# Kernel optimization log

Measured on AMD Instinct MI355X. Metric: run time of the kernel, lower is better.

The kernel has to match this reference:

```python
import jax, jax.numpy as jnp
import numpy as np

B, L = 4, 2048
D_MODEL, D_STATE, D_CONV, N_BLOCKS = 128, 16, 8, 6
EXPAND = 2
D_INNER = EXPAND * D_MODEL          # 256
DT_RANK = (D_MODEL + 15) // 16      # 8
CONV_K = 7                          # pre_conv kernel


def setup_inputs() -> dict:
    key = jax.random.key(0)
    ks = jax.random.split(key, 10)
    f = lambda k, s: jax.random.normal(k, s, jnp.float32)
    sc = 0.02
    A_init = jnp.broadcast_to(
        jnp.log(jnp.arange(1, D_STATE + 1, dtype=jnp.float32)),
        (N_BLOCKS, D_INNER, D_STATE)) + 0.0
    return {
        "x": f(ks[0], (B, L, 1)),
        "pre_conv_w": f(ks[1], (D_MODEL, 1, CONV_K)) * sc,
        "pre_conv_b": jnp.zeros((D_MODEL,), jnp.float32),
        "ln_w": jnp.ones((N_BLOCKS, D_MODEL), jnp.float32),
        "ln_b": jnp.zeros((N_BLOCKS, D_MODEL), jnp.float32),
        "W_in": f(ks[2], (N_BLOCKS, 2 * D_INNER, D_MODEL)) * sc,
        "conv_w": f(ks[3], (N_BLOCKS, D_INNER, 1, D_CONV)) * sc,  # depthwise OIH
        "conv_b": jnp.zeros((N_BLOCKS, D_INNER), jnp.float32),
        "W_x": f(ks[4], (N_BLOCKS, DT_RANK + 2 * D_STATE, D_INNER)) * sc,
        "W_dt": f(ks[5], (N_BLOCKS, D_INNER, DT_RANK)) * sc,
        "b_dt": jnp.full((N_BLOCKS, D_INNER), -4.6, jnp.float32),  # softplus ~ 0.01
        "A_log": A_init,
        "D_skip": jnp.ones((N_BLOCKS, D_INNER), jnp.float32),
        "W_out": f(ks[6], (N_BLOCKS, D_MODEL, D_INNER)) * sc,
        "out_w": f(ks[7], (1, D_MODEL)) * sc,
        "out_b": jnp.zeros((1,), jnp.float32),
    }


def _layernorm(x, w, b, eps=1e-5):
    m = jnp.mean(x, axis=-1, keepdims=True)
    v = jnp.mean(jnp.square(x - m), axis=-1, keepdims=True)
    return (x - m) * jax.lax.rsqrt(v + eps) * w + b


def _mamba(x, W_in, cw, cb, W_x, W_dt, b_dt, A_log, D_skip, W_out):
    # x: (B, L, D_MODEL)
    xz = jnp.einsum('bld,ed->ble', x, W_in)            # (B,L,2E)
    xi, z = jnp.split(xz, 2, axis=-1)
    # depthwise causal conv over time
    xc = jax.lax.conv_general_dilated(
        xi.transpose(0, 2, 1), cw, window_strides=(1,),
        padding=[(D_CONV - 1, 0)],
        dimension_numbers=('NCH', 'OIH', 'NCH'),
        feature_group_count=D_INNER) + cb[None, :, None]
    xc = jax.nn.silu(xc).transpose(0, 2, 1)            # (B,L,E)
    dbl = jnp.einsum('ble,re->blr', xc, W_x)
    dt = dbl[..., :DT_RANK]
    Bm = dbl[..., DT_RANK:DT_RANK + D_STATE]           # (B,L,N)
    Cm = dbl[..., DT_RANK + D_STATE:]                  # (B,L,N)
    delta = jax.nn.softplus(jnp.einsum('blr,er->ble', dt, W_dt) + b_dt)
    A = -jnp.exp(A_log)                                # (E,N)

    def step(h, inp):
        d, b, c, u = inp                               # (B,E),(B,N),(B,N),(B,E)
        h = h * jnp.exp(d[..., None] * A) + (d * u)[..., None] * b[:, None, :]
        return h, jnp.einsum('ben,bn->be', h, c)

    h0 = jnp.zeros((x.shape[0], D_INNER, D_STATE), x.dtype)
    xs = (delta.transpose(1, 0, 2), Bm.transpose(1, 0, 2),
          Cm.transpose(1, 0, 2), xc.transpose(1, 0, 2))
    _, ys = jax.lax.scan(step, h0, xs)                 # ys: (L,B,E)
    y = ys.transpose(1, 0, 2) + D_skip * xc
    y = y * jax.nn.silu(z)
    return jnp.einsum('ble,de->bld', y, W_out)


def reference(x, pre_conv_w, pre_conv_b, ln_w, ln_b, W_in, conv_w, conv_b,
              W_x, W_dt, b_dt, A_log, D_skip, W_out, out_w, out_b):
    # pre_conv (1 -> d_model), SAME padding, then exact GELU
    h = jax.lax.conv_general_dilated(
        x.transpose(0, 2, 1), pre_conv_w, window_strides=(1,),
        padding=[(CONV_K // 2, CONV_K // 2)],
        dimension_numbers=('NCH', 'OIH', 'NCH')) + pre_conv_b[None, :, None]
    h = jax.nn.gelu(h, approximate=False).transpose(0, 2, 1)  # (B,L,D)

    def block(carry, p):
        lw, lb, Wi, cw, cb, Wx, Wdt, bdt, Alog, Dsk, Wo = p
        y = _mamba(_layernorm(carry, lw, lb), Wi, cw, cb, Wx, Wdt, bdt, Alog, Dsk, Wo)
        return carry + y, None                         # dropout is identity (eval)

    h, _ = jax.lax.scan(block, h, (ln_w, ln_b, W_in, conv_w, conv_b,
                                   W_x, W_dt, b_dt, A_log, D_skip, W_out))
    return (jnp.einsum('bld,od->blo', h, out_w) + out_b)[..., 0]  # (B,L)
```

## Files before the change

### kernel.cpp

```cpp
#include <hip/hip_runtime.h>
#include <hip/hip_bf16.h>
#include <math.h>

#define BB 4
#define LL 2048
#define DM 128
#define DI 256
#define DS 16
#define DTR 8
#define NB 6
#define KPRE 7
#define KC 8
#define NC 64
#define CT 32
#define BL (BB*LL)
#define SU 4

typedef __attribute__((ext_vector_type(8))) short short8v;
typedef __attribute__((ext_vector_type(4))) float f32x4;

__global__ void k_preconv_gelu(const float* __restrict__ x,
                               const float* __restrict__ w,
                               const float* __restrict__ bias,
                               float* __restrict__ h,
                               const float* __restrict__ Wi,
                               const float* __restrict__ Wo,
                               __hip_bfloat16* __restrict__ wi,
                               __hip_bfloat16* __restrict__ wo) {
    int tid = blockIdx.x * blockDim.x + threadIdx.x;
    int d = tid & (DM - 1);
    int l = (tid >> 7) & (LL - 1);
    int b = tid >> 18;
    float acc = bias[d];
#pragma unroll
    for (int k = 0; k < KPRE; ++k) {
        int pos = l + k - 3;
        float xv = (pos >= 0 && pos < LL) ? x[b * LL + pos] : 0.f;
        acc = fmaf(xv, w[d * KPRE + k], acc);
    }
    h[tid] = 0.5f * acc * (1.f + erff(acc * 0.70710678118654752f));
    if (tid < NB * 2 * DI * DM) wi[tid] = __float2bfloat16(Wi[tid]);
    if (tid < NB * DM * DI)     wo[tid] = __float2bfloat16(Wo[tid]);
}

__global__ __launch_bounds__(256) void k_ln_gemm1(const float* __restrict__ h,
                                                  const float* __restrict__ lw,
                                                  const float* __restrict__ lb,
                                                  const __hip_bfloat16* __restrict__ W,
                                                  float* __restrict__ xz) {
    __shared__ __hip_bfloat16 As[128 * 128];
    int wave = threadIdx.x >> 6;
    int lane = threadIdx.x & 63;
    int mBase = blockIdx.x * 128;
    int nBase = blockIdx.y * 128;
    for (int it = 0; it < 32; ++it) {
        int row = wave * 32 + it;
        int t = mBase + row;
        float v0 = h[t * DM + lane];
        float v1 = h[t * DM + lane + 64];
        float s = v0 + v1;
#pragma unroll
        for (int off = 32; off; off >>= 1) s += __shfl_xor(s, off);
        float mean = s * (1.f / 128.f);
        float d0 = v0 - mean, d1 = v1 - mean;
        float q = d0 * d0 + d1 * d1;
#pragma unroll
        for (int off = 32; off; off >>= 1) q += __shfl_xor(q, off);
        float rstd = rsqrtf(q * (1.f / 128.f) + 1e-5f);
        int sw = (row & 7) << 3;
        As[row * 128 + (lane ^ sw)]        = __float2bfloat16(d0 * rstd * lw[lane] + lb[lane]);
        As[row * 128 + ((lane + 64) ^ sw)] = __float2bfloat16(d1 * rstd * lw[lane + 64] + lb[lane + 64]);
    }
    __syncthreads();
    int wm = wave & 1, wn = wave >> 1;
    int r  = lane & 15;
    int kh = lane >> 4;
    f32x4 acc[4][4] = {};
    for (int k0 = 0; k0 < DM; k0 += 32) {
        short8v af[4], bf[4];
#pragma unroll
        for (int i = 0; i < 4; ++i) {
            int row = wm * 64 + i * 16 + r;
            int cbk = (k0 >> 3) + kh;
            af[i] = *(const short8v*)&As[row * 128 + ((cbk ^ (row & 7)) << 3)];
            bf[i] = *(const short8v*)&W[(size_t)(nBase + wn * 64 + i * 16 + r) * DM + k0 + kh * 8];
        }
#pragma unroll
        for (int i = 0; i < 4; ++i)
#pragma unroll
            for (int j = 0; j < 4; ++j)
                acc[i][j] = __builtin_amdgcn_mfma_f32_16x16x32_bf16(af[i], bf[j], acc[i][j], 0, 0, 0);
    }
#pragma unroll
    for (int i = 0; i < 4; ++i)
#pragma unroll
        for (int j = 0; j < 4; ++j)
#pragma unroll
            for (int rg = 0; rg < 4; ++rg) {
                size_t off = (size_t)(mBase + wm * 64 + i * 16 + kh * 4 + rg) * (2 * DI)
                           + nBase + wn * 64 + j * 16 + r;
                xz[off] = acc[i][j][rg];
            }
}

__global__ __launch_bounds__(256) void k_gemm2_mfma(const __hip_bfloat16* __restrict__ A,
                                                    const __hip_bfloat16* __restrict__ W,
                                                    float* __restrict__ C) {
    int wave = threadIdx.x >> 6;
    int lane = threadIdx.x & 63;
    int wm = wave & 1, wn = wave >> 1;
    int mBase = blockIdx.x * 128 + wm * 64;
    int nBase = wn * 64;
    int r  = lane & 15;
    int kh = lane >> 4;
    f32x4 acc[4][4] = {};
    for (int k0 = 0; k0 < DI; k0 += 32) {
        short8v af[4], bf[4];
#pragma unroll
        for (int i = 0; i < 4; ++i) {
            af[i] = *(const short8v*)&A[(size_t)(mBase + i * 16 + r) * DI + k0 + kh * 8];
            bf[i] = *(const short8v*)&W[(size_t)(nBase + i * 16 + r) * DI + k0 + kh * 8];
        }
#pragma unroll
        for (int i = 0; i < 4; ++i)
#pragma unroll
            for (int j = 0; j < 4; ++j)
                acc[i][j] = __builtin_amdgcn_mfma_f32_16x16x32_bf16(af[i], bf[j], acc[i][j], 0, 0, 0);
    }
#pragma unroll
    for (int i = 0; i < 4; ++i)
#pragma unroll
        for (int j = 0; j < 4; ++j)
#pragma unroll
            for (int rg = 0; rg < 4; ++rg) {
                size_t off = (size_t)(mBase + i * 16 + kh * 4 + rg) * DM + nBase + j * 16 + r;
                C[off] += acc[i][j][rg];
            }
}

__global__ __launch_bounds__(256) void k_conv_wx(const float* __restrict__ xz,
                                                 const float* __restrict__ cw,
                                                 const float* __restrict__ cbs,
                                                 const float* __restrict__ Wx,
                                                 const float* __restrict__ Wdt,
                                                 const float* __restrict__ bdt,
                                                 float* __restrict__ xc,
                                                 float* __restrict__ BC,
                                                 float* __restrict__ delta) {
    int lane = threadIdx.x & 63;
    int t = blockIdx.x * 4 + (threadIdx.x >> 6);
    int tl = t & (LL - 1);
    int b = t >> 11;
    float xv[4];
#pragma unroll
    for (int j = 0; j < 4; ++j) {
        int e = lane + 64 * j;
        float4 cw0 = *(const float4*)&cw[e * KC];
        float4 cw1 = *(const float4*)&cw[e * KC + 4];
        float wts[8] = {cw0.x, cw0.y, cw0.z, cw0.w, cw1.x, cw1.y, cw1.z, cw1.w};
        float acc = cbs[e];
#pragma unroll
        for (int k = 0; k < KC; ++k) {
            int pos = tl + k - (KC - 1);
            float v = (pos >= 0) ? xz[((size_t)(b * LL + pos) << 9) + e] : 0.f;
            acc = fmaf(v, wts[k], acc);
        }
        xv[j] = acc / (1.f + __expf(-acc));
        xc[((size_t)t << 8) + e] = xv[j];
    }
    float dt[8];
    float bcv = 0.f;
#pragma unroll
    for (int o = 0; o < 40; ++o) {
        const float* w = &Wx[o * DI];
        float s = xv[0] * w[lane];
        s = fmaf(xv[1], w[lane + 64], s);
        s = fmaf(xv[2], w[lane + 128], s);
        s = fmaf(xv[3], w[lane + 192], s);
#pragma unroll
        for (int off = 32; off; off >>= 1) s += __shfl_xor(s, off);
        if (o < 8) dt[o] = s;
        else if (lane == o - 8) bcv = s;
    }
    if (lane < 32) BC[((size_t)t << 5) + lane] = bcv;
#pragma unroll
    for (int j = 0; j < 4; ++j) {
        int e = lane + 64 * j;
        float s = bdt[e];
#pragma unroll
        for (int r = 0; r < 8; ++r) s = fmaf(dt[r], Wdt[e * 8 + r], s);
        delta[((size_t)t << 8) + e] = fmaxf(s, 0.f) + log1pf(__expf(-fabsf(s)));
    }
}

__global__ __launch_bounds__(256) void k_scan1(const float* __restrict__ delta,
                                               const float* __restrict__ xc,
                                               const float* __restrict__ BC,
                                               const float* __restrict__ A_log,
                                               float* __restrict__ P,
                                               float* __restrict__ hend) {
    int blk = blockIdx.x;
    int eg = blk & 3;
    int c = (blk >> 2) & (NC - 1);
    int b = blk >> 8;
    int tid = threadIdx.x;
    int e = eg * 64 + (tid >> 2);
    int ng = tid & 3;
    float4 al = *(const float4*)&A_log[e * DS + 4 * ng];
    float Aen[4] = {-__expf(al.x), -__expf(al.y), -__expf(al.z), -__expf(al.w)};
    float h[4] = {}, Pl[4] = {1.f, 1.f, 1.f, 1.f};
    int base = b * LL + c * CT;
    const float* dp = delta + (size_t)base * DI + e;
    const float* up = xc + (size_t)base * DI + e;
    const float* bp = BC + (size_t)base * 32 + 4 * ng;
    for (int l0 = 0; l0 < CT; l0 += SU) {
        float d[SU], u[SU];
        float4 bm[SU];
#pragma unroll
        for (int j = 0; j < SU; ++j) {
            d[j]  = dp[(l0 + j) * DI];
            u[j]  = up[(l0 + j) * DI];
            bm[j] = *(const float4*)&bp[(l0 + j) * 32];
        }
#pragma unroll
        for (int j = 0; j < SU; ++j) {
            float du = d[j] * u[j];
            float a0 = __expf(d[j] * Aen[0]);
            float a1 = __expf(d[j] * Aen[1]);
            float a2 = __expf(d[j] * Aen[2]);
            float a3 = __expf(d[j] * Aen[3]);
            h[0] = fmaf(h[0], a0, du * bm[j].x);
            h[1] = fmaf(h[1], a1, du * bm[j].y);
            h[2] = fmaf(h[2], a2, du * bm[j].z);
            h[3] = fmaf(h[3], a3, du * bm[j].w);
            Pl[0] *= a0; Pl[1] *= a1; Pl[2] *= a2; Pl[3] *= a3;
        }
    }
    size_t oidx = (((size_t)(b * NC + c)) * DI + e) * DS + 4 * ng;
    *(float4*)&P[oidx]    = make_float4(Pl[0], Pl[1], Pl[2], Pl[3]);
    *(float4*)&hend[oidx] = make_float4(h[0], h[1], h[2], h[3]);
}

__global__ void k_scan_carry(const float* __restrict__ P,
                             const float* __restrict__ hend,
                             float* __restrict__ hin) {
    int tid = blockIdx.x * blockDim.x + threadIdx.x;
    int n = tid & 15;
    int e = (tid >> 4) & 255;
    int b = tid >> 12;
    float carry = 0.f;
    for (int c = 0; c < NC; ++c) {
        size_t idx = (((size_t)(b * NC + c)) * DI + e) * DS + n;
        hin[idx] = carry;
        carry = fmaf(P[idx], carry, hend[idx]);
    }
}

__global__ __launch_bounds__(256) void k_scan3(const float* __restrict__ delta,
                                               const float* __restrict__ xc,
                                               const float* __restrict__ BC,
                                               const float* __restrict__ A_log,
                                               const float* __restrict__ hin,
                                               const float* __restrict__ xz,
                                               const float* __restrict__ Dsk,
                                               __hip_bfloat16* __restrict__ y) {
    int blk = blockIdx.x;
    int eg = blk & 3;
    int c = (blk >> 2) & (NC - 1);
    int b = blk >> 8;
    int tid = threadIdx.x;
    int e = eg * 64 + (tid >> 2);
    int ng = tid & 3;
    float4 al = *(const float4*)&A_log[e * DS + 4 * ng];
    float Aen[4] = {-__expf(al.x), -__expf(al.y), -__expf(al.z), -__expf(al.w)};
    float dsk = Dsk[e];
    size_t hidx = (((size_t)(b * NC + c)) * DI + e) * DS + 4 * ng;
    float4 h4 = *(const float4*)&hin[hidx];
    float h[4] = {h4.x, h4.y, h4.z, h4.w};
    int base = b * LL + c * CT;
    const float* dp = delta + (size_t)base * DI + e;
    const float* up = xc + (size_t)base * DI + e;
    const float* bp = BC + (size_t)base * 32 + 4 * ng;
    const float* zp = xz + ((size_t)base << 9) + DI + e;
    __hip_bfloat16* yp = y + (size_t)base * DI + e;
    for (int l0 = 0; l0 < CT; l0 += SU) {
        float d[SU], u[SU], zv[SU];
        float4 bm[SU], cm[SU];
#pragma unroll
        for (int j = 0; j < SU; ++j) {
            d[j]  = dp[(l0 + j) * DI];
            u[j]  = up[(l0 + j) * DI];
            bm[j] = *(const float4*)&bp[(l0 + j) * 32];
            cm[j] = *(const float4*)&bp[(l0 + j) * 32 + 16];
            zv[j] = zp[(size_t)(l0 + j) << 9];
        }
#pragma unroll
        for (int j = 0; j < SU; ++j) {
            float du = d[j] * u[j];
            float a0 = __expf(d[j] * Aen[0]);
            float a1 = __expf(d[j] * Aen[1]);
            float a2 = __expf(d[j] * Aen[2]);
            float a3 = __expf(d[j] * Aen[3]);
            h[0] = fmaf(h[0], a0, du * bm[j].x);
            h[1] = fmaf(h[1], a1, du * bm[j].y);
            h[2] = fmaf(h[2], a2, du * bm[j].z);
            h[3] = fmaf(h[3], a3, du * bm[j].w);
            float yc = h[0] * cm[j].x;
            yc = fmaf(h[1], cm[j].y, yc);
            yc = fmaf(h[2], cm[j].z, yc);
            yc = fmaf(h[3], cm[j].w, yc);
            yc += __shfl_xor(yc, 1);
            yc += __shfl_xor(yc, 2);
            if (ng == 0) {
                float z = zv[j];
                float val = (yc + dsk * u[j]) * (z / (1.f + __expf(-z)));
                yp[(l0 + j) * DI] = __float2bfloat16(val);
            }
        }
    }
}

__global__ void k_out(const float* __restrict__ h,
                      const float* __restrict__ ow,
                      const float* __restrict__ ob,
                      float* __restrict__ out) {
    int t = blockIdx.x * 4 + (threadIdx.x >> 6);
    int lane = threadIdx.x & 63;
    float s = h[t * DM + lane] * ow[lane] + h[t * DM + lane + 64] * ow[lane + 64];
#pragma unroll
    for (int off = 32; off; off >>= 1) s += __shfl_xor(s, off);
    if (lane == 0) out[t] = s + ob[0];
}

extern "C" void kernel_launch(void* const* d_in, const int* in_sizes, int n_in,
                              void* d_out, int out_size, void* d_ws, size_t ws_size,
                              hipStream_t stream) {
    (void)in_sizes; (void)n_in; (void)out_size; (void)ws_size;
    const float* x      = (const float*)d_in[0];
    const float* pcw    = (const float*)d_in[1];
    const float* pcb    = (const float*)d_in[2];
    const float* ln_w   = (const float*)d_in[3];
    const float* ln_b   = (const float*)d_in[4];
    const float* W_in   = (const float*)d_in[5];
    const float* conv_w = (const float*)d_in[6];
    const float* conv_b = (const float*)d_in[7];
    const float* W_x    = (const float*)d_in[8];
    const float* W_dt   = (const float*)d_in[9];
    const float* b_dt   = (const float*)d_in[10];
    const float* A_log  = (const float*)d_in[11];
    const float* D_skip = (const float*)d_in[12];
    const float* W_out  = (const float*)d_in[13];
    const float* out_w  = (const float*)d_in[14];
    const float* out_b  = (const float*)d_in[15];

    float* ws    = (float*)d_ws;
    float* h     = ws;
    float* xz    = h     + (size_t)BL * DM;
    float* xc    = xz    + (size_t)BL * 2 * DI;
    float* BC    = xc    + (size_t)BL * DI;
    float* delta = BC    + (size_t)BL * 2 * DS;
    float* P     = delta + (size_t)BL * DI;
    float* hend  = P     + (size_t)BB * NC * DI * DS;
    float* hin   = hend  + (size_t)BB * NC * DI * DS;
    __hip_bfloat16* y_bf  = (__hip_bfloat16*)(hin + (size_t)BB * NC * DI * DS);
    __hip_bfloat16* wi_bf = y_bf  + (size_t)BL * DI;
    __hip_bfloat16* wo_bf = wi_bf + (size_t)NB * 2 * DI * DM;

    k_preconv_gelu<<<(BB * LL * DM) / 256, 256, 0, stream>>>(
        x, pcw, pcb, h, W_in, W_out, wi_bf, wo_bf);

    for (int blk = 0; blk < NB; ++blk) {
        k_ln_gemm1<<<dim3(BL / 128, (2 * DI) / 128), 256, 0, stream>>>(
            h, ln_w + blk * DM, ln_b + blk * DM, wi_bf + (size_t)blk * 2 * DI * DM, xz);
        k_conv_wx<<<BL / 4, 256, 0, stream>>>(
            xz, conv_w + (size_t)blk * DI * KC, conv_b + blk * DI,
            W_x + (size_t)blk * 40 * DI, W_dt + (size_t)blk * DI * DTR,
            b_dt + blk * DI, xc, BC, delta);
        k_scan1<<<BB * NC * 4, 256, 0, stream>>>(
            delta, xc, BC, A_log + (size_t)blk * DI * DS, P, hend);
        k_scan_carry<<<(BB * DI * DS) / 256, 256, 0, stream>>>(P, hend, hin);
        k_scan3<<<BB * NC * 4, 256, 0, stream>>>(
            delta, xc, BC, A_log + (size_t)blk * DI * DS, hin, xz,
            D_skip + blk * DI, y_bf);
        k_gemm2_mfma<<<BL / 128, 256, 0, stream>>>(
            y_bf, wo_bf + (size_t)blk * DM * DI, h);
    }

    k_out<<<BL / 4, 256, 0, stream>>>(h, out_w, out_b, (float*)d_out);
}
```

Measured before the change: 686.9 us.

## Fuse conv/x-proj into chunk scan pass and out-projection GEMM into scan pass

Merges the depthwise conv + x-projection kernel with the first chunked-scan pass, keeping xc, delta and B/C for a 32-step chunk in shared memory so the scan reads them from there instead of from global memory. Also fuses the output projection GEMM into the second scan pass: y is staged in shared memory as bf16 and multiplied by W_out with MFMA, removing the y buffer and a launch. Blocks now cover a whole chunk with 1024 threads, so only 256 blocks launch per kernel, which lowers parallelism and occupancy compared with the previous 1024-block scan launches.

```diff
diff --git a/kernel.cpp b/kernel.cpp
--- a/kernel.cpp
+++ b/kernel.cpp
@@ -103,124 +103,92 @@
             }
 }
 
-__global__ __launch_bounds__(256) void k_gemm2_mfma(const __hip_bfloat16* __restrict__ A,
-                                                    const __hip_bfloat16* __restrict__ W,
-                                                    float* __restrict__ C) {
+__global__ __launch_bounds__(1024) void k_conv_scan1(const float* __restrict__ xz,
+                                                     const float* __restrict__ cw,
+                                                     const float* __restrict__ cbs,
+                                                     const float* __restrict__ Wx,
+                                                     const float* __restrict__ Wdt,
+                                                     const float* __restrict__ bdt,
+                                                     const float* __restrict__ A_log,
+                                                     float* __restrict__ xc,
+                                                     float* __restrict__ BC,
+                                                     float* __restrict__ delta,
+                                                     float* __restrict__ P,
+                                                     float* __restrict__ hend) {
+    __shared__ float xc_s[CT][DI];
+    __shared__ float dl_s[CT][DI];
+    __shared__ float bc_s[CT][32];
+    int blk = blockIdx.x;
+    int c = blk & (NC - 1);
+    int b = blk >> 6;
     int wave = threadIdx.x >> 6;
     int lane = threadIdx.x & 63;
-    int wm = wave & 1, wn = wave >> 1;
-    int mBase = blockIdx.x * 128 + wm * 64;
-    int nBase = wn * 64;
-    int r  = lane & 15;
-    int kh = lane >> 4;
-    f32x4 acc[4][4] = {};
-    for (int k0 = 0; k0 < DI; k0 += 32) {
-        short8v af[4], bf[4];
-#pragma unroll
-        for (int i = 0; i < 4; ++i) {
-            af[i] = *(const short8v*)&A[(size_t)(mBase + i * 16 + r) * DI + k0 + kh * 8];
-            bf[i] = *(const short8v*)&W[(size_t)(nBase + i * 16 + r) * DI + k0 + kh * 8];
-        }
-#pragma unroll
-        for (int i = 0; i < 4; ++i)
-#pragma unroll
-            for (int j = 0; j < 4; ++j)
-                acc[i][j] = __builtin_amdgcn_mfma_f32_16x16x32_bf16(af[i], bf[j], acc[i][j], 0, 0, 0);
-    }
-#pragma unroll
-    for (int i = 0; i < 4; ++i)
-#pragma unroll
-        for (int j = 0; j < 4; ++j)
-#pragma unroll
-            for (int rg = 0; rg < 4; ++rg) {
-                size_t off = (size_t)(mBase + i * 16 + kh * 4 + rg) * DM + nBase + j * 16 + r;
-                C[off] += acc[i][j][rg];
+    for (int i = 0; i < 2; ++i) {
+        int lt = wave * 2 + i;
+        int tl = c * CT + lt;
+        int t  = b * LL + tl;
+        float xv[4];
+#pragma unroll
+        for (int j = 0; j < 4; ++j) {
+            int e = lane + 64 * j;
+            float4 cw0 = *(const float4*)&cw[e * KC];
+            float4 cw1 = *(const float4*)&cw[e * KC + 4];
+            float wts[8] = {cw0.x, cw0.y, cw0.z, cw0.w, cw1.x, cw1.y, cw1.z, cw1.w};
+            float acc = cbs[e];
+#pragma unroll
+            for (int k = 0; k < KC; ++k) {
+                int pos = tl + k - (KC - 1);
+                float v = (pos >= 0) ? xz[((size_t)(b * LL + pos) << 9) + e] : 0.f;
+                acc = fmaf(v, wts[k], acc);
             }
-}
-
-__global__ __launch_bounds__(256) void k_conv_wx(const float* __restrict__ xz,
-                                                 const float* __restrict__ cw,
-                                                 const float* __restrict__ cbs,
-                                                 const float* __restrict__ Wx,
-                                                 const float* __restrict__ Wdt,
-                                                 const float* __restrict__ bdt,
-                                                 float* __restrict__ xc,
-                                                 float* __restrict__ BC,
-                                                 float* __restrict__ delta) {
-    int lane = threadIdx.x & 63;
-    int t = blockIdx.x * 4 + (threadIdx.x >> 6);
-    int tl = t & (LL - 1);
-    int b = t >> 11;
-    float xv[4];
-#pragma unroll
-    for (int j = 0; j < 4; ++j) {
-        int e = lane + 64 * j;
-        float4 cw0 = *(const float4*)&cw[e * KC];
-        float4 cw1 = *(const float4*)&cw[e * KC + 4];
-        float wts[8] = {cw0.x, cw0.y, cw0.z, cw0.w, cw1.x, cw1.y, cw1.z, cw1.w};
-        float acc = cbs[e];
-#pragma unroll
-        for (int k = 0; k < KC; ++k) {
-            int pos = tl + k - (KC - 1);
-            float v = (pos >= 0) ? xz[((size_t)(b * LL + pos) << 9) + e] : 0.f;
-            acc = fmaf(v, wts[k], acc);
-        }
-        xv[j] = acc / (1.f + __expf(-acc));
-        xc[((size_t)t << 8) + e] = xv[j];
-    }
-    float dt[8];
-    float bcv = 0.f;
-#pragma unroll
-    for (int o = 0; o < 40; ++o) {
-        const float* w = &Wx[o * DI];
-        float s = xv[0] * w[lane];
-        s = fmaf(xv[1], w[lane + 64], s);
-        s = fmaf(xv[2], w[lane + 128], s);
-        s = fmaf(xv[3], w[lane + 192], s);
-#pragma unroll
-        for (int off = 32; off; off >>= 1) s += __shfl_xor(s, off);
-        if (o < 8) dt[o] = s;
-        else if (lane == o - 8) bcv = s;
-    }
-    if (lane < 32) BC[((size_t)t << 5) + lane] = bcv;
-#pragma unroll
-    for (int j = 0; j < 4; ++j) {
-        int e = lane + 64 * j;
-        float s = bdt[e];
-#pragma unroll
-        for (int r = 0; r < 8; ++r) s = fmaf(dt[r], Wdt[e * 8 + r], s);
-        delta[((size_t)t << 8) + e] = fmaxf(s, 0.f) + log1pf(__expf(-fabsf(s)));
-    }
-}
-
-__global__ __launch_bounds__(256) void k_scan1(const float* __restrict__ delta,
-                                               const float* __restrict__ xc,
-                                               const float* __restrict__ BC,
-                                               const float* __restrict__ A_log,
-                                               float* __restrict__ P,
-                                               float* __restrict__ hend) {
-    int blk = blockIdx.x;
-    int eg = blk & 3;
-    int c = (blk >> 2) & (NC - 1);
-    int b = blk >> 8;
-    int tid = threadIdx.x;
-    int e = eg * 64 + (tid >> 2);
-    int ng = tid & 3;
+            float sv = acc / (1.f + __expf(-acc));
+            xv[j] = sv;
+            xc_s[lt][e] = sv;
+            xc[((size_t)t << 8) + e] = sv;
+        }
+        float dt8[8];
+        float bcv = 0.f;
+#pragma unroll
+        for (int o = 0; o < 40; ++o) {
+            const float* w = &Wx[o * DI];
+            float s = xv[0] * w[lane];
+            s = fmaf(xv[1], w[lane + 64], s);
+            s = fmaf(xv[2], w[lane + 128], s);
+            s = fmaf(xv[3], w[lane + 192], s);
+#pragma unroll
+            for (int off = 32; off; off >>= 1) s += __shfl_xor(s, off);
+            if (o < 8) dt8[o] = s;
+            else if (lane == o - 8) bcv = s;
+        }
+        if (lane < 32) {
+            bc_s[lt][lane] = bcv;
+            BC[((size_t)t << 5) + lane] = bcv;
+        }
+#pragma unroll
+        for (int j = 0; j < 4; ++j) {
+            int e = lane + 64 * j;
+            float s = bdt[e];
+#pragma unroll
+            for (int r = 0; r < 8; ++r) s = fmaf(dt8[r], Wdt[e * 8 + r], s);
+            float dv = fmaxf(s, 0.f) + log1pf(__expf(-fabsf(s)));
+            dl_s[lt][e] = dv;
+            delta[((size_t)t << 8) + e] = dv;
+        }
+    }
+    __syncthreads();
+    int e = threadIdx.x >> 2;
+    int ng = threadIdx.x & 3;
     float4 al = *(const float4*)&A_log[e * DS + 4 * ng];
     float Aen[4] = {-__expf(al.x), -__expf(al.y), -__expf(al.z), -__expf(al.w)};
-    float h[4] = {}, Pl[4] = {1.f, 1.f, 1.f, 1.f};
-    int base = b * LL + c * CT;
-    const float* dp = delta + (size_t)base * DI + e;
-    const float* up = xc + (size_t)base * DI + e;
-    const float* bp = BC + (size_t)base * 32 + 4 * ng;
+    float hh[4] = {}, Pl[4] = {1.f, 1.f, 1.f, 1.f};
     for (int l0 = 0; l0 < CT; l0 += SU) {
         float d[SU], u[SU];
         float4 bm[SU];
 #pragma unroll
         for (int j = 0; j < SU; ++j) {
-            d[j]  = dp[(l0 + j) * DI];
-            u[j]  = up[(l0 + j) * DI];
-            bm[j] = *(const float4*)&bp[(l0 + j) * 32];
+            d[j]  = dl_s[l0 + j][e];
+            u[j]  = xc_s[l0 + j][e];
+            bm[j] = *(const float4*)&bc_s[l0 + j][4 * ng];
         }
 #pragma unroll
         for (int j = 0; j < SU; ++j) {
@@ -229,16 +197,16 @@
             float a1 = __expf(d[j] * Aen[1]);
             float a2 = __expf(d[j] * Aen[2]);
             float a3 = __expf(d[j] * Aen[3]);
-            h[0] = fmaf(h[0], a0, du * bm[j].x);
-            h[1] = fmaf(h[1], a1, du * bm[j].y);
-            h[2] = fmaf(h[2], a2, du * bm[j].z);
-            h[3] = fmaf(h[3], a3, du * bm[j].w);
+            hh[0] = fmaf(hh[0], a0, du * bm[j].x);
+            hh[1] = fmaf(hh[1], a1, du * bm[j].y);
+            hh[2] = fmaf(hh[2], a2, du * bm[j].z);
+            hh[3] = fmaf(hh[3], a3, du * bm[j].w);
             Pl[0] *= a0; Pl[1] *= a1; Pl[2] *= a2; Pl[3] *= a3;
         }
     }
     size_t oidx = (((size_t)(b * NC + c)) * DI + e) * DS + 4 * ng;
     *(float4*)&P[oidx]    = make_float4(Pl[0], Pl[1], Pl[2], Pl[3]);
-    *(float4*)&hend[oidx] = make_float4(h[0], h[1], h[2], h[3]);
+    *(float4*)&hend[oidx] = make_float4(hh[0], hh[1], hh[2], hh[3]);
 }
 
 __global__ void k_scan_carry(const float* __restrict__ P,
@@ -256,33 +224,32 @@
     }
 }
 
-__global__ __launch_bounds__(256) void k_scan3(const float* __restrict__ delta,
-                                               const float* __restrict__ xc,
-                                               const float* __restrict__ BC,
-                                               const float* __restrict__ A_log,
-                                               const float* __restrict__ hin,
-                                               const float* __restrict__ xz,
-                                               const float* __restrict__ Dsk,
-                                               __hip_bfloat16* __restrict__ y) {
+__global__ __launch_bounds__(1024) void k_scan3_gemm2(const float* __restrict__ delta,
+                                                      const float* __restrict__ xc,
+                                                      const float* __restrict__ BC,
+                                                      const float* __restrict__ A_log,
+                                                      const float* __restrict__ hin,
+                                                      const float* __restrict__ xz,
+                                                      const float* __restrict__ Dsk,
+                                                      const __hip_bfloat16* __restrict__ Wo,
+                                                      float* __restrict__ hout) {
+    __shared__ __hip_bfloat16 y_s[CT][DI + 8];
     int blk = blockIdx.x;
-    int eg = blk & 3;
-    int c = (blk >> 2) & (NC - 1);
-    int b = blk >> 8;
-    int tid = threadIdx.x;
-    int e = eg * 64 + (tid >> 2);
-    int ng = tid & 3;
+    int c = blk & (NC - 1);
+    int b = blk >> 6;
+    int e = threadIdx.x >> 2;
+    int ng = threadIdx.x & 3;
     float4 al = *(const float4*)&A_log[e * DS + 4 * ng];
     float Aen[4] = {-__expf(al.x), -__expf(al.y), -__expf(al.z), -__expf(al.w)};
     float dsk = Dsk[e];
     size_t hidx = (((size_t)(b * NC + c)) * DI + e) * DS + 4 * ng;
     float4 h4 = *(const float4*)&hin[hidx];
-    float h[4] = {h4.x, h4.y, h4.z, h4.w};
+    float hh[4] = {h4.x, h4.y, h4.z, h4.w};
     int base = b * LL + c * CT;
     const float* dp = delta + (size_t)base * DI + e;
     const float* up = xc + (size_t)base * DI + e;
     const float* bp = BC + (size_t)base * 32 + 4 * ng;
     const float* zp = xz + ((size_t)base << 9) + DI + e;
-    __hip_bfloat16* yp = y + (size_t)base * DI + e;
     for (int l0 = 0; l0 < CT; l0 += SU) {
         float d[SU], u[SU], zv[SU];
         float4 bm[SU], cm[SU];
@@ -301,22 +268,41 @@
             float a1 = __expf(d[j] * Aen[1]);
             float a2 = __expf(d[j] * Aen[2]);
             float a3 = __expf(d[j] * Aen[3]);
-            h[0] = fmaf(h[0], a0, du * bm[j].x);
-            h[1] = fmaf(h[1], a1, du * bm[j].y);
-            h[2] = fmaf(h[2], a2, du * bm[j].z);
-            h[3] = fmaf(h[3], a3, du * bm[j].w);
-            float yc = h[0] * cm[j].x;
-            yc = fmaf(h[1], cm[j].y, yc);
-            yc = fmaf(h[2], cm[j].z, yc);
-            yc = fmaf(h[3], cm[j].w, yc);
+            hh[0] = fmaf(hh[0], a0, du * bm[j].x);
+            hh[1] = fmaf(hh[1], a1, du * bm[j].y);
+            hh[2] = fmaf(hh[2], a2, du * bm[j].z);
+            hh[3] = fmaf(hh[3], a3, du * bm[j].w);
+            float yc = hh[0] * cm[j].x;
+            yc = fmaf(hh[1], cm[j].y, yc);
+            yc = fmaf(hh[2], cm[j].z, yc);
+            yc = fmaf(hh[3], cm[j].w, yc);
             yc += __shfl_xor(yc, 1);
             yc += __shfl_xor(yc, 2);
             if (ng == 0) {
                 float z = zv[j];
                 float val = (yc + dsk * u[j]) * (z / (1.f + __expf(-z)));
-                yp[(l0 + j) * DI] = __float2bfloat16(val);
+                y_s[l0 + j][e] = __float2bfloat16(val);
             }
         }
+    }
+    __syncthreads();
+    int wave = threadIdx.x >> 6;
+    int lane = threadIdx.x & 63;
+    int mt = wave >> 3;
+    int nt = wave & 7;
+    int r  = lane & 15;
+    int kh = lane >> 4;
+    f32x4 acc = {};
+    for (int k0 = 0; k0 < DI; k0 += 32) {
+        short8v af = *(const short8v*)&y_s[mt * 16 + r][k0 + kh * 8];
+        short8v bf = *(const short8v*)&Wo[(size_t)(nt * 16 + r) * DI + k0 + kh * 8];
+        acc = __builtin_amdgcn_mfma_f32_16x16x32_bf16(af, bf, acc, 0, 0, 0);
+    }
+#pragma unroll
+    for (int rg = 0; rg < 4; ++rg) {
+        int row = mt * 16 + kh * 4 + rg;
+        size_t off = (size_t)(base + row) * DM + nt * 16 + r;
+        hout[off] += acc[rg];
     }
 }
 
@@ -362,8 +348,7 @@
     float* P     = delta + (size_t)BL * DI;
     float* hend  = P     + (size_t)BB * NC * DI * DS;
     float* hin   = hend  + (size_t)BB * NC * DI * DS;
-    __hip_bfloat16* y_bf  = (__hip_bfloat16*)(hin + (size_t)BB * NC * DI * DS);
-    __hip_bfloat16* wi_bf = y_bf  + (size_t)BL * DI;
+    __hip_bfloat16* wi_bf = (__hip_bfloat16*)(hin + (size_t)BB * NC * DI * DS);
     __hip_bfloat16* wo_bf = wi_bf + (size_t)NB * 2 * DI * DM;
 
     k_preconv_gelu<<<(BB * LL * DM) / 256, 256, 0, stream>>>(
@@ -372,18 +357,15 @@
     for (int blk = 0; blk < NB; ++blk) {
         k_ln_gemm1<<<dim3(BL / 128, (2 * DI) / 128), 256, 0, stream>>>(
             h, ln_w + blk * DM, ln_b + blk * DM, wi_bf + (size_t)blk * 2 * DI * DM, xz);
-        k_conv_wx<<<BL / 4, 256, 0, stream>>>(
+        k_conv_scan1<<<BB * NC, 1024, 0, stream>>>(
             xz, conv_w + (size_t)blk * DI * KC, conv_b + blk * DI,
             W_x + (size_t)blk * 40 * DI, W_dt + (size_t)blk * DI * DTR,
-            b_dt + blk * DI, xc, BC, delta);
-        k_scan1<<<BB * NC * 4, 256, 0, stream>>>(
-            delta, xc, BC, A_log + (size_t)blk * DI * DS, P, hend);
+            b_dt + blk * DI, A_log + (size_t)blk * DI * DS,
+            xc, BC, delta, P, hend);
         k_scan_carry<<<(BB * DI * DS) / 256, 256, 0, stream>>>(P, hend, hin);
-        k_scan3<<<BB * NC * 4, 256, 0, stream>>>(
+        k_scan3_gemm2<<<BB * NC, 1024, 0, stream>>>(
             delta, xc, BC, A_log + (size_t)blk * DI * DS, hin, xz,
-            D_skip + blk * DI, y_bf);
-        k_gemm2_mfma<<<BL / 128, 256, 0, stream>>>(
-            y_bf, wo_bf + (size_t)blk * DM * DI, h);
+            D_skip + blk * DI, wo_bf + (size_t)blk * DM * DI, h);
     }
 
     k_out<<<BL / 4, 256, 0, stream>>>(h, out_w, out_b, (float*)d_out);
```

Result: slower. 1.940 ms (+182.4%).
